# Performance work log

Hardware: AMD Instinct MI355X
Metric: run time of the kernel (lower is better)

The kernel has to match this reference:

```python
import jax, jax.numpy as jnp
import numpy as np

B, C, H, W = 4, 64, 128, 128
EPS = 1e-5


def setup_inputs() -> dict:
    key = jax.random.key(0)
    ks = jax.random.split(key, 6)
    x = jax.random.normal(ks[0], (B, C, H, W), jnp.float32)
    W1 = jax.random.normal(ks[1], (C, C), jnp.float32) * 0.1
    b1 = jnp.zeros((C,), jnp.float32)
    W2 = jax.random.normal(ks[2], (C, C), jnp.float32) * 0.1
    b2 = jnp.zeros((C,), jnp.float32)
    Wc = jax.random.normal(ks[3], (C, C, 3, 3), jnp.float32) * 0.05
    bn_w = jnp.ones((C,), jnp.float32)
    bn_b = jnp.zeros((C,), jnp.float32)
    gamma = jax.random.normal(ks[4], (1,), jnp.float32) * 0.5
    return dict(x=x, W1=W1, b1=b1, W2=W2, b2=b2, Wc=Wc, bn_w=bn_w, bn_b=bn_b, gamma=gamma)


def reference(x, W1, b1, W2, b2, Wc, bn_w, bn_b, gamma):
    b, c, h, w = x.shape
    # feat_h: [B,W,C,H] flattened to [C, B*W, H] (exact torch .view semantics)
    feat_h = x.transpose(0, 3, 1, 2).reshape(c, b * w, h)
    # feat_w: [B,H,C,W] flattened to [C, B*H, W]
    feat_w = x.transpose(0, 2, 1, 3).reshape(c, b * h, w)
    # avg-pool over W -> [B,C,H] -> [C,H,B]; 1x1 conv == channel mix on dim0
    enc_h = jnp.einsum('oi,ihb->ohb', W1, x.mean(axis=3).transpose(1, 2, 0)) + b1[:, None, None]  # [C,H,B]
    enc_w = jnp.einsum('oi,iwb->owb', W2, x.mean(axis=2).transpose(1, 2, 0)) + b2[:, None, None]  # [C,W,B]
    # energy_h: [C, B*W, B*W]
    energy_h = jnp.matmul(feat_h, jnp.tile(enc_h, (1, 1, w)))
    rel_h = jax.nn.softmax(energy_h, axis=-1)
    aug_h = jnp.matmul(rel_h, feat_h).reshape(b, w, c, h).transpose(0, 2, 3, 1)  # [B,C,H,W]
    # energy_w: [C, B*H, B*H]
    energy_w = jnp.matmul(feat_w, jnp.tile(enc_w, (1, 1, h)))
    rel_w = jax.nn.softmax(energy_w, axis=-1)
    aug_w = jnp.matmul(rel_w, feat_w).reshape(b, h, c, w).transpose(0, 2, 1, 3)  # [B,C,H,W]
    out = gamma * (aug_h + aug_w) + x
    # 3x3 conv (no bias) + BatchNorm2d (training-mode batch stats) + ReLU
    y = jax.lax.conv_general_dilated(out, Wc, (1, 1), 'SAME',
                                     dimension_numbers=('NCHW', 'OIHW', 'NCHW'))
    mean = y.mean(axis=(0, 2, 3), keepdims=True)
    var = y.var(axis=(0, 2, 3), keepdims=True)
    y = (y - mean) * jax.lax.rsqrt(var + EPS)
    y = y * bn_w[None, :, None, None] + bn_b[None, :, None, None]
    return jax.nn.relu(y)
```

## Files before the change

### kernel.cpp

```cpp
#include <hip/hip_runtime.h>
#include <math.h>

#define BDIM 4
#define CDIM 64
#define HDIM 128
#define WDIM 128
#define PLANE (HDIM*WDIM)
#define CHW (CDIM*PLANE)

typedef unsigned short ushort_t;
typedef short short8 __attribute__((ext_vector_type(8)));
typedef float floatx4 __attribute__((ext_vector_type(4)));

__device__ inline unsigned int pack_bf16(float lo, float hi) {
  unsigned int ul = __float_as_uint(lo);
  unsigned int uh = __float_as_uint(hi);
  unsigned int rl = (ul + 0x7FFFu + ((ul >> 16) & 1u)) >> 16;
  unsigned int rh = (uh + 0x7FFFu + ((uh >> 16) & 1u)) >> 16;
  return (rh << 16) | (rl & 0xFFFFu);
}

__global__ __launch_bounds__(256) void k1_T_rowmean(const float* __restrict__ x,
                                                    float* __restrict__ T,
                                                    float* __restrict__ xmw) {
  int bid = blockIdx.x;
  int b = bid >> 7, h = bid & 127;
  int t = threadIdx.x;
  int wid = t >> 6, lane = t & 63;
  const float* xp = x + (size_t)b * CHW + h * WDIM;
  float tr[4] = {0,0,0,0}, ur[4] = {0,0,0,0};
#pragma unroll
  for (int cc = 0; cc < 16; cc++) {
    int c = wid * 16 + cc;
    int k = cc & 3;
    float v0 = xp[c * PLANE + lane];
    float v1 = xp[c * PLANE + lane + 64];
    tr[k] += v0; ur[k] += v1;
    float s = v0 + v1;
#pragma unroll
    for (int off = 32; off; off >>= 1) s += __shfl_xor(s, off);
    if (lane == 0) xmw[(b * CDIM + c) * HDIM + h] = s * (1.f / WDIM);
  }
  __shared__ float4 pt[4][128];
  pt[wid][lane]      = make_float4(tr[0], tr[1], tr[2], tr[3]);
  pt[wid][lane + 64] = make_float4(ur[0], ur[1], ur[2], ur[3]);
  __syncthreads();
  if (t < 128) {
    float4 a = pt[0][t], bb = pt[1][t], cvec = pt[2][t], d = pt[3][t];
    float4 s = make_float4(a.x + bb.x + cvec.x + d.x, a.y + bb.y + cvec.y + d.y,
                           a.z + bb.z + cvec.z + d.z, a.w + bb.w + cvec.w + d.w);
    ((float4*)T)[(b * HDIM + h) * WDIM + t] = s;
  }
}

__global__ void k2_colmean(const float* __restrict__ x, float* __restrict__ xmh) {
  int bid = blockIdx.x;
  int b = bid >> 6, c = bid & 63;
  int t = threadIdx.x;
  int tw = t & 127, th2 = t >> 7;
  const float* xp = x + (size_t)(b * CDIM + c) * PLANE;
  float s = 0.f;
  for (int h = th2 * 64; h < th2 * 64 + 64; h++) s += xp[h * WDIM + tw];
  __shared__ float sh[256];
  sh[t] = s;
  __syncthreads();
  if (t < 128) xmh[(b * CDIM + c) * WDIM + t] = (sh[t] + sh[t + 128]) * (1.f / HDIM);
}

__global__ void k3_enc(const float* __restrict__ W1, const float* __restrict__ bias1,
                       const float* __restrict__ W2, const float* __restrict__ bias2,
                       const float* __restrict__ xmw, const float* __restrict__ xmh,
                       float* __restrict__ ench, float* __restrict__ encw) {
  int bid = blockIdx.x;
  int t = threadIdx.x;
  int o = t >> 2, bb = t & 3;
  if (bid < HDIM) {
    int h = bid;
    float s = bias1[o];
    for (int i = 0; i < CDIM; i++) s += W1[o * CDIM + i] * xmw[(bb * CDIM + i) * HDIM + h];
    ench[(o * HDIM + h) * 4 + bb] = s;
  } else {
    int w = bid - HDIM;
    float s = bias2[o];
    for (int i = 0; i < CDIM; i++) s += W2[o * CDIM + i] * xmh[(bb * CDIM + i) * WDIM + w];
    encw[(o * WDIM + w) * 4 + bb] = s;
  }
}

__global__ __launch_bounds__(256) void k4_probs(const float* __restrict__ x,
                                                const float* __restrict__ ench,
                                                const float* __restrict__ encw,
                                                float* __restrict__ Ph,
                                                float* __restrict__ Pw) {
  __shared__ float plane[HDIM * WDIM];
  int bid = blockIdx.x;
  int b = bid >> 6, c = bid & 63;
  int t = threadIdx.x;
  const float* xp = x + (size_t)(b * CDIM + c) * PLANE;
#pragma unroll 4
  for (int j = 0; j < 64; j++) {
    int idx = j * 256 + t;
    int row = idx >> 7, col = idx & 127;
    plane[row * WDIM + (col ^ (row & 31))] = xp[idx];
  }
  __syncthreads();
  int half = t >> 7, p = t & 127;
  int c2 = (b * HDIM + p) >> 3;
  float e0 = 0, e1 = 0, e2 = 0, e3 = 0;
  if (half == 0) {
    const float4* E = (const float4*)ench + c2 * HDIM;
    for (int h = 0; h < HDIM; h++) {
      float v = plane[h * WDIM + (p ^ (h & 31))];
      float4 e = E[h];
      e0 += v * e.x; e1 += v * e.y; e2 += v * e.z; e3 += v * e.w;
    }
  } else {
    const float4* E = (const float4*)encw + c2 * WDIM;
    for (int w = 0; w < WDIM; w++) {
      float v = plane[p * WDIM + (w ^ (p & 31))];
      float4 e = E[w];
      e0 += v * e.x; e1 += v * e.y; e2 += v * e.z; e3 += v * e.w;
    }
  }
  float m = fmaxf(fmaxf(e0, e1), fmaxf(e2, e3));
  float p0 = expf(e0 - m), p1 = expf(e1 - m), p2 = expf(e2 - m), p3 = expf(e3 - m);
  float sc = 1.f / ((p0 + p1 + p2 + p3) * 128.f);
  float4* dst = (half == 0) ? (float4*)Ph : (float4*)Pw;
  dst[c2 * 512 + (p & 7) * 64 + c] = make_float4(p0 * sc, p1 * sc, p2 * sc, p3 * sc);
}

__global__ void k4b_groups(const float* __restrict__ T, float* __restrict__ Gh,
                           float* __restrict__ Gw) {
  int c2 = blockIdx.x;
  int t = threadIdx.x;
  int b = c2 >> 4;
  int w0 = (c2 & 15) * 8;
  const float4* T4 = (const float4*)T;
  float4 s = make_float4(0, 0, 0, 0);
#pragma unroll
  for (int dw = 0; dw < 8; dw++) {
    float4 v = T4[(b * HDIM + t) * WDIM + w0 + dw];
    s.x += v.x; s.y += v.y; s.z += v.z; s.w += v.w;
  }
  ((float4*)Gh)[c2 * HDIM + t] = s;
  float4 s2 = make_float4(0, 0, 0, 0);
#pragma unroll
  for (int dh = 0; dh < 8; dh++) {
    float4 v = T4[(b * HDIM + w0 + dh) * WDIM + t];
    s2.x += v.x; s2.y += v.y; s2.z += v.z; s2.w += v.w;
  }
  ((float4*)Gw)[c2 * WDIM + t] = s2;
}

__global__ __launch_bounds__(256) void k5_out(const float* __restrict__ x,
                                              const float* __restrict__ Ph,
                                              const float* __restrict__ Pw,
                                              const float* __restrict__ Gh,
                                              const float* __restrict__ Gw,
                                              const float* __restrict__ gamma,
                                              float* __restrict__ outb) {
  int bid = blockIdx.x;
  int hq = bid & 3, c = (bid >> 2) & 63, b = bid >> 8;
  int t = threadIdx.x;
  int tw = t & 127, th2 = t >> 7;
  float g = gamma[0];
  int c2h = (b * HDIM + tw) >> 3;
  float4 ph = ((const float4*)Ph)[c2h * 512 + (tw & 7) * 64 + c];
  const float* xp = x + (size_t)(b * CDIM + c) * PLANE;
  float* op = outb + (size_t)(b * CDIM + c) * PLANE;
#pragma unroll 4
  for (int j = 0; j < 16; j++) {
    int h = hq * 32 + j * 2 + th2;
    int c2w = (b * HDIM + h) >> 3;
    float4 pw = ((const float4*)Pw)[c2w * 512 + (h & 7) * 64 + c];
    float4 gh = ((const float4*)Gh)[c2h * HDIM + h];
    float4 gw = ((const float4*)Gw)[c2w * WDIM + tw];
    float val = ph.x * gh.x + ph.y * gh.y + ph.z * gh.z + ph.w * gh.w
              + pw.x * gw.x + pw.y * gw.y + pw.z * gw.z + pw.w * gw.w;
    op[h * WDIM + tw] = fmaf(g, val, xp[h * WDIM + tw]);
  }
}

__global__ void k6_prep(const float* __restrict__ Wc, ushort_t* __restrict__ afrag) {
  int idx = blockIdx.x * 256 + threadIdx.x;
  if (idx >= 4608) return;
  int lane = idx & 63;
  int m = (idx >> 6) & 3;
  int chunk = (idx >> 8) & 1;
  int tap = idx >> 9;
  int dh = tap / 3, dw = tap % 3;
  int o = m * 16 + (lane & 15);
  int ib = chunk * 32 + (lane >> 4) * 8;
  unsigned int d[4];
#pragma unroll
  for (int j = 0; j < 4; j++) {
    float lo = Wc[((size_t)(o * CDIM + ib + 2 * j) * 3 + dh) * 3 + dw];
    float hi = Wc[((size_t)(o * CDIM + ib + 2 * j + 1) * 3 + dh) * 3 + dw];
    d[j] = pack_bf16(lo, hi);
  }
  uint4* dst = (uint4*)afrag + idx;
  *dst = make_uint4(d[0], d[1], d[2], d[3]);
}

__global__ __launch_bounds__(512) void k6_conv(const float* __restrict__ outb,
                                               const ushort_t* __restrict__ afrag,
                                               float* __restrict__ yb) {
  __shared__ uint4 lds_in[3 * 130 * 4];
  int bid = blockIdx.x;
  int b = bid >> 7, h0 = bid & 127;
  int t = threadIdx.x;
  int lane = t & 63, wv = t >> 6;
  int w0 = wv * 16;
  const float* inb = outb + (size_t)b * CHW;

  floatx4 acc[4];
#pragma unroll
  for (int m = 0; m < 4; m++) acc[m] = (floatx4){0.f, 0.f, 0.f, 0.f};

  for (int chunk = 0; chunk < 2; chunk++) {
    int i0 = chunk * 32;
    __syncthreads();
#pragma unroll
    for (int k = 0; k < 4; k++) {
      int gid = k * 512 + t;
      if (gid < 1560) {
        int wlp = gid % 130;
        int rest = gid / 130;
        int g = rest & 3, lr = rest >> 2;
        int h = h0 - 1 + lr, wl = wlp - 1;
        unsigned int d0 = 0, d1 = 0, d2 = 0, d3 = 0;
        if (h >= 0 && h < HDIM && wl >= 0 && wl < WDIM) {
          const float* sp = inb + (size_t)(i0 + g * 8) * PLANE + h * WDIM + wl;
          float v0 = sp[0], v1 = sp[PLANE], v2 = sp[2 * PLANE], v3 = sp[3 * PLANE];
          float v4 = sp[4 * PLANE], v5 = sp[5 * PLANE], v6 = sp[6 * PLANE], v7 = sp[7 * PLANE];
          d0 = pack_bf16(v0, v1); d1 = pack_bf16(v2, v3);
          d2 = pack_bf16(v4, v5); d3 = pack_bf16(v6, v7);
        }
        int pg = g ^ ((wlp >> 1) & 3);
        lds_in[(lr * 130 + wlp) * 4 + pg] = make_uint4(d0, d1, d2, d3);
      }
    }
    __syncthreads();
#pragma unroll
    for (int tap = 0; tap < 9; tap++) {
      int lr = tap / 3, dw = tap % 3;
      int wlp = w0 + (lane & 15) + dw;
      int pg = (lane >> 4) ^ ((wlp >> 1) & 3);
      short8 bf = *(const short8*)&lds_in[(lr * 130 + wlp) * 4 + pg];
      const short8* ap = (const short8*)afrag + (size_t)((tap * 2 + chunk) * 4) * 64 + lane;
#pragma unroll
      for (int m = 0; m < 4; m++) {
        short8 a = ap[m * 64];
        acc[m] = __builtin_amdgcn_mfma_f32_16x16x32_bf16(a, bf, acc[m], 0, 0, 0);
      }
    }
  }
  int col = lane & 15, rg = lane >> 4;
#pragma unroll
  for (int m = 0; m < 4; m++) {
#pragma unroll
    for (int j = 0; j < 4; j++) {
      int o = m * 16 + rg * 4 + j;
      yb[((size_t)(b * CDIM + o) * HDIM + h0) * WDIM + w0 + col] = acc[m][j];
    }
  }
}

__global__ __launch_bounds__(512) void k7a_stats(const float* __restrict__ yb,
                                                 float* __restrict__ part) {
  int bid = blockIdx.x;
  int t = threadIdx.x;
  const float4* yp = (const float4*)(yb + (size_t)bid * PLANE);
  float s = 0.f, ss = 0.f;
  for (int r = t; r < PLANE / 4; r += 512) {
    float4 v = yp[r];
    s  += v.x + v.y + v.z + v.w;
    ss += v.x * v.x + v.y * v.y + v.z * v.z + v.w * v.w;
  }
#pragma unroll
  for (int off = 32; off; off >>= 1) { s += __shfl_xor(s, off); ss += __shfl_xor(ss, off); }
  __shared__ float sh[16];
  int wid = t >> 6;
  if ((t & 63) == 0) { sh[wid] = s; sh[8 + wid] = ss; }
  __syncthreads();
  if (t == 0) {
    s = 0.f; ss = 0.f;
#pragma unroll
    for (int wv = 0; wv < 8; wv++) { s += sh[wv]; ss += sh[8 + wv]; }
    part[bid] = s;
    part[256 + bid] = ss;
  }
}

__global__ void k7b_finalize(const float* __restrict__ part, float* __restrict__ stats) {
  int o = threadIdx.x;
  float s = 0.f, ss = 0.f;
#pragma unroll
  for (int b = 0; b < BDIM; b++) { s += part[b * 64 + o]; ss += part[256 + b * 64 + o]; }
  float n = (float)(BDIM * PLANE);
  float m = s / n;
  float var = ss / n - m * m;
  stats[o] = m;
  stats[64 + o] = rsqrtf(var + 1e-5f);
}

__global__ void k8_norm(const float* __restrict__ yb, const float* __restrict__ stats,
                        const float* __restrict__ bnw, const float* __restrict__ bnb,
                        float* __restrict__ out) {
  int idx = blockIdx.x * 256 + threadIdx.x;
  int c = (idx >> 12) & 63;
  float4 v = ((const float4*)yb)[idx];
  float m = stats[c], rs = stats[64 + c], w = bnw[c], bb = bnb[c];
  v.x = fmaxf(0.f, (v.x - m) * rs * w + bb);
  v.y = fmaxf(0.f, (v.y - m) * rs * w + bb);
  v.z = fmaxf(0.f, (v.z - m) * rs * w + bb);
  v.w = fmaxf(0.f, (v.w - m) * rs * w + bb);
  ((float4*)out)[idx] = v;
}

extern "C" void kernel_launch(void* const* d_in, const int* in_sizes, int n_in,
                              void* d_out, int out_size, void* d_ws, size_t ws_size,
                              hipStream_t stream) {
  const float* x     = (const float*)d_in[0];
  const float* W1    = (const float*)d_in[1];
  const float* b1    = (const float*)d_in[2];
  const float* W2    = (const float*)d_in[3];
  const float* b2    = (const float*)d_in[4];
  const float* Wc    = (const float*)d_in[5];
  const float* bnw   = (const float*)d_in[6];
  const float* bnb   = (const float*)d_in[7];
  const float* gamma = (const float*)d_in[8];
  float* out = (float*)d_out;

  float* ws   = (float*)d_ws;
  float* T    = ws;
  float* xmw  = T    + 262144;
  float* xmh  = xmw  + 32768;
  float* ench = xmh  + 32768;
  float* encw = ench + 32768;
  float* Ph   = encw + 32768;
  float* Pw   = Ph   + 131072;
  float* Gh   = Pw   + 131072;
  float* Gw   = Gh   + 32768;
  float* outb = Gw   + 32768;
  float* yb   = outb + 4194304;
  float* part = yb   + 4194304;
  float* stats= part + 512;
  ushort_t* afrag = (ushort_t*)(stats + 128);

  k6_prep     <<<18, 256, 0, stream>>>(Wc, afrag);
  k1_T_rowmean<<<512, 256, 0, stream>>>(x, T, xmw);
  k2_colmean  <<<256, 256, 0, stream>>>(x, xmh);
  k3_enc      <<<256, 256, 0, stream>>>(W1, b1, W2, b2, xmw, xmh, ench, encw);
  k4_probs    <<<256, 256, 0, stream>>>(x, ench, encw, Ph, Pw);
  k4b_groups  <<<64, 128, 0, stream>>>(T, Gh, Gw);
  k5_out      <<<1024, 256, 0, stream>>>(x, Ph, Pw, Gh, Gw, gamma, outb);
  k6_conv     <<<512, 512, 0, stream>>>(outb, afrag, yb);
  k7a_stats   <<<256, 512, 0, stream>>>(yb, part);
  k7b_finalize<<<1, 64, 0, stream>>>(part, stats);
  k8_norm     <<<4096, 256, 0, stream>>>(yb, stats, bnw, bnb, out);
}
```

Before: 171.0 us.

## Fuse attention output into conv loader, BN stats into conv epilogue, merge small kernels

The residual attention output is no longer written to a buffer. The conv input loader now recomputes gamma*(Ph·Gh+Pw·Gw)+x directly while staging bf16 tiles, which removes a full 16 MB write and read. BatchNorm statistics are gathered in the conv epilogue with shuffles, shared atomics and global atomics, which drops the separate stats and finalize kernels; the encoder and group-sum kernels are also merged and k4_probs splits its reductions across 512 threads. In exchange the conv loader does more redundant arithmetic and gathers per halo element, and the float atomics make the statistics order nondeterministic.

```diff
diff --git a/kernel.cpp b/kernel.cpp
--- a/kernel.cpp
+++ b/kernel.cpp
@@ -67,122 +67,103 @@
   if (t < 128) xmh[(b * CDIM + c) * WDIM + t] = (sh[t] + sh[t + 128]) * (1.f / HDIM);
 }
 
-__global__ void k3_enc(const float* __restrict__ W1, const float* __restrict__ bias1,
-                       const float* __restrict__ W2, const float* __restrict__ bias2,
-                       const float* __restrict__ xmw, const float* __restrict__ xmh,
-                       float* __restrict__ ench, float* __restrict__ encw) {
-  int bid = blockIdx.x;
-  int t = threadIdx.x;
-  int o = t >> 2, bb = t & 3;
-  if (bid < HDIM) {
-    int h = bid;
-    float s = bias1[o];
-    for (int i = 0; i < CDIM; i++) s += W1[o * CDIM + i] * xmw[(bb * CDIM + i) * HDIM + h];
-    ench[(o * HDIM + h) * 4 + bb] = s;
-  } else {
-    int w = bid - HDIM;
-    float s = bias2[o];
-    for (int i = 0; i < CDIM; i++) s += W2[o * CDIM + i] * xmh[(bb * CDIM + i) * WDIM + w];
-    encw[(o * WDIM + w) * 4 + bb] = s;
-  }
-}
-
-__global__ __launch_bounds__(256) void k4_probs(const float* __restrict__ x,
+__global__ void k3_enc_groups(const float* __restrict__ W1, const float* __restrict__ bias1,
+                              const float* __restrict__ W2, const float* __restrict__ bias2,
+                              const float* __restrict__ xmw, const float* __restrict__ xmh,
+                              const float* __restrict__ T,
+                              float* __restrict__ ench, float* __restrict__ encw,
+                              float* __restrict__ Gh, float* __restrict__ Gw) {
+  int bid = blockIdx.x;
+  int t = threadIdx.x;
+  if (bid < 256) {
+    int o = t >> 2, bb = t & 3;
+    if (bid < HDIM) {
+      int h = bid;
+      float s = bias1[o];
+      for (int i = 0; i < CDIM; i++) s += W1[o * CDIM + i] * xmw[(bb * CDIM + i) * HDIM + h];
+      ench[(o * HDIM + h) * 4 + bb] = s;
+    } else {
+      int w = bid - HDIM;
+      float s = bias2[o];
+      for (int i = 0; i < CDIM; i++) s += W2[o * CDIM + i] * xmh[(bb * CDIM + i) * WDIM + w];
+      encw[(o * WDIM + w) * 4 + bb] = s;
+    }
+  } else if (t < 128) {
+    int c2 = bid - 256;
+    int b = c2 >> 4;
+    int w0 = (c2 & 15) * 8;
+    const float4* T4 = (const float4*)T;
+    float4 s = make_float4(0, 0, 0, 0);
+#pragma unroll
+    for (int dw = 0; dw < 8; dw++) {
+      float4 v = T4[(b * HDIM + t) * WDIM + w0 + dw];
+      s.x += v.x; s.y += v.y; s.z += v.z; s.w += v.w;
+    }
+    ((float4*)Gh)[c2 * HDIM + t] = s;
+    float4 s2 = make_float4(0, 0, 0, 0);
+#pragma unroll
+    for (int dh = 0; dh < 8; dh++) {
+      float4 v = T4[(b * HDIM + w0 + dh) * WDIM + t];
+      s2.x += v.x; s2.y += v.y; s2.z += v.z; s2.w += v.w;
+    }
+    ((float4*)Gw)[c2 * WDIM + t] = s2;
+  }
+}
+
+__global__ __launch_bounds__(512) void k4_probs(const float* __restrict__ x,
                                                 const float* __restrict__ ench,
                                                 const float* __restrict__ encw,
                                                 float* __restrict__ Ph,
                                                 float* __restrict__ Pw) {
   __shared__ float plane[HDIM * WDIM];
+  __shared__ float4 esh[512];
   int bid = blockIdx.x;
   int b = bid >> 6, c = bid & 63;
   int t = threadIdx.x;
   const float* xp = x + (size_t)(b * CDIM + c) * PLANE;
 #pragma unroll 4
-  for (int j = 0; j < 64; j++) {
-    int idx = j * 256 + t;
+  for (int j = 0; j < 32; j++) {
+    int idx = j * 512 + t;
     int row = idx >> 7, col = idx & 127;
     plane[row * WDIM + (col ^ (row & 31))] = xp[idx];
   }
   __syncthreads();
-  int half = t >> 7, p = t & 127;
+  int q = t >> 7, p = t & 127;
+  int branch = q >> 1, seg = q & 1;
   int c2 = (b * HDIM + p) >> 3;
   float e0 = 0, e1 = 0, e2 = 0, e3 = 0;
-  if (half == 0) {
+  if (branch == 0) {
     const float4* E = (const float4*)ench + c2 * HDIM;
-    for (int h = 0; h < HDIM; h++) {
+    for (int h = seg * 64; h < seg * 64 + 64; h++) {
       float v = plane[h * WDIM + (p ^ (h & 31))];
       float4 e = E[h];
       e0 += v * e.x; e1 += v * e.y; e2 += v * e.z; e3 += v * e.w;
     }
   } else {
     const float4* E = (const float4*)encw + c2 * WDIM;
-    for (int w = 0; w < WDIM; w++) {
+    for (int w = seg * 64; w < seg * 64 + 64; w++) {
       float v = plane[p * WDIM + (w ^ (p & 31))];
       float4 e = E[w];
       e0 += v * e.x; e1 += v * e.y; e2 += v * e.z; e3 += v * e.w;
     }
   }
-  float m = fmaxf(fmaxf(e0, e1), fmaxf(e2, e3));
-  float p0 = expf(e0 - m), p1 = expf(e1 - m), p2 = expf(e2 - m), p3 = expf(e3 - m);
-  float sc = 1.f / ((p0 + p1 + p2 + p3) * 128.f);
-  float4* dst = (half == 0) ? (float4*)Ph : (float4*)Pw;
-  dst[c2 * 512 + (p & 7) * 64 + c] = make_float4(p0 * sc, p1 * sc, p2 * sc, p3 * sc);
-}
-
-__global__ void k4b_groups(const float* __restrict__ T, float* __restrict__ Gh,
-                           float* __restrict__ Gw) {
-  int c2 = blockIdx.x;
-  int t = threadIdx.x;
-  int b = c2 >> 4;
-  int w0 = (c2 & 15) * 8;
-  const float4* T4 = (const float4*)T;
-  float4 s = make_float4(0, 0, 0, 0);
-#pragma unroll
-  for (int dw = 0; dw < 8; dw++) {
-    float4 v = T4[(b * HDIM + t) * WDIM + w0 + dw];
-    s.x += v.x; s.y += v.y; s.z += v.z; s.w += v.w;
-  }
-  ((float4*)Gh)[c2 * HDIM + t] = s;
-  float4 s2 = make_float4(0, 0, 0, 0);
-#pragma unroll
-  for (int dh = 0; dh < 8; dh++) {
-    float4 v = T4[(b * HDIM + w0 + dh) * WDIM + t];
-    s2.x += v.x; s2.y += v.y; s2.z += v.z; s2.w += v.w;
-  }
-  ((float4*)Gw)[c2 * WDIM + t] = s2;
-}
-
-__global__ __launch_bounds__(256) void k5_out(const float* __restrict__ x,
-                                              const float* __restrict__ Ph,
-                                              const float* __restrict__ Pw,
-                                              const float* __restrict__ Gh,
-                                              const float* __restrict__ Gw,
-                                              const float* __restrict__ gamma,
-                                              float* __restrict__ outb) {
-  int bid = blockIdx.x;
-  int hq = bid & 3, c = (bid >> 2) & 63, b = bid >> 8;
-  int t = threadIdx.x;
-  int tw = t & 127, th2 = t >> 7;
-  float g = gamma[0];
-  int c2h = (b * HDIM + tw) >> 3;
-  float4 ph = ((const float4*)Ph)[c2h * 512 + (tw & 7) * 64 + c];
-  const float* xp = x + (size_t)(b * CDIM + c) * PLANE;
-  float* op = outb + (size_t)(b * CDIM + c) * PLANE;
-#pragma unroll 4
-  for (int j = 0; j < 16; j++) {
-    int h = hq * 32 + j * 2 + th2;
-    int c2w = (b * HDIM + h) >> 3;
-    float4 pw = ((const float4*)Pw)[c2w * 512 + (h & 7) * 64 + c];
-    float4 gh = ((const float4*)Gh)[c2h * HDIM + h];
-    float4 gw = ((const float4*)Gw)[c2w * WDIM + tw];
-    float val = ph.x * gh.x + ph.y * gh.y + ph.z * gh.z + ph.w * gh.w
-              + pw.x * gw.x + pw.y * gw.y + pw.z * gw.z + pw.w * gw.w;
-    op[h * WDIM + tw] = fmaf(g, val, xp[h * WDIM + tw]);
-  }
-}
-
-__global__ void k6_prep(const float* __restrict__ Wc, ushort_t* __restrict__ afrag) {
+  esh[t] = make_float4(e0, e1, e2, e3);
+  __syncthreads();
+  if (seg == 0) {
+    float4 o = esh[t + 128];
+    e0 += o.x; e1 += o.y; e2 += o.z; e3 += o.w;
+    float m = fmaxf(fmaxf(e0, e1), fmaxf(e2, e3));
+    float p0 = __expf(e0 - m), p1 = __expf(e1 - m), p2 = __expf(e2 - m), p3 = __expf(e3 - m);
+    float sc = 1.f / ((p0 + p1 + p2 + p3) * 128.f);
+    float4* dst = (branch == 0) ? (float4*)Ph : (float4*)Pw;
+    dst[c2 * 512 + (p & 7) * 64 + c] = make_float4(p0 * sc, p1 * sc, p2 * sc, p3 * sc);
+  }
+}
+
+__global__ void k6_prep(const float* __restrict__ Wc, ushort_t* __restrict__ afrag,
+                        float* __restrict__ part) {
   int idx = blockIdx.x * 256 + threadIdx.x;
+  if (idx < 128) part[idx] = 0.f;
   if (idx >= 4608) return;
   int lane = idx & 63;
   int m = (idx >> 6) & 3;
@@ -202,16 +183,30 @@
   *dst = make_uint4(d[0], d[1], d[2], d[3]);
 }
 
-__global__ __launch_bounds__(512) void k6_conv(const float* __restrict__ outb,
+__global__ __launch_bounds__(512) void k6_conv(const float* __restrict__ x,
+                                               const float* __restrict__ Ph,
+                                               const float* __restrict__ Pw,
+                                               const float* __restrict__ Gh,
+                                               const float* __restrict__ Gw,
+                                               const float* __restrict__ gamma,
                                                const ushort_t* __restrict__ afrag,
-                                               float* __restrict__ yb) {
+                                               float* __restrict__ yb,
+                                               float* __restrict__ part) {
   __shared__ uint4 lds_in[3 * 130 * 4];
+  __shared__ float sh_s[64], sh_ss[64];
   int bid = blockIdx.x;
   int b = bid >> 7, h0 = bid & 127;
   int t = threadIdx.x;
   int lane = t & 63, wv = t >> 6;
   int w0 = wv * 16;
-  const float* inb = outb + (size_t)b * CHW;
+  const float* xb = x + (size_t)b * CHW;
+  const float4* Ph4 = (const float4*)Ph;
+  const float4* Pw4 = (const float4*)Pw;
+  const float4* Gh4 = (const float4*)Gh;
+  const float4* Gw4 = (const float4*)Gw;
+  float gm = gamma[0];
+
+  if (t < 64) { sh_s[t] = 0.f; sh_ss[t] = 0.f; }
 
   floatx4 acc[4];
 #pragma unroll
@@ -230,11 +225,24 @@
         int h = h0 - 1 + lr, wl = wlp - 1;
         unsigned int d0 = 0, d1 = 0, d2 = 0, d3 = 0;
         if (h >= 0 && h < HDIM && wl >= 0 && wl < WDIM) {
-          const float* sp = inb + (size_t)(i0 + g * 8) * PLANE + h * WDIM + wl;
-          float v0 = sp[0], v1 = sp[PLANE], v2 = sp[2 * PLANE], v3 = sp[3 * PLANE];
-          float v4 = sp[4 * PLANE], v5 = sp[5 * PLANE], v6 = sp[6 * PLANE], v7 = sp[7 * PLANE];
-          d0 = pack_bf16(v0, v1); d1 = pack_bf16(v2, v3);
-          d2 = pack_bf16(v4, v5); d3 = pack_bf16(v6, v7);
+          int c0 = i0 + g * 8;
+          int c2h = (b * HDIM + wl) >> 3;
+          int c2w = (b * HDIM + h) >> 3;
+          float4 gh4 = Gh4[c2h * HDIM + h];
+          float4 gw4 = Gw4[c2w * WDIM + wl];
+          const float4* php = Ph4 + c2h * 512 + (wl & 7) * 64 + c0;
+          const float4* pwp = Pw4 + c2w * 512 + (h & 7) * 64 + c0;
+          const float* xpp = xb + (size_t)c0 * PLANE + h * WDIM + wl;
+          float v[8];
+#pragma unroll
+          for (int j = 0; j < 8; j++) {
+            float4 ph = php[j], pw = pwp[j];
+            float val = ph.x * gh4.x + ph.y * gh4.y + ph.z * gh4.z + ph.w * gh4.w
+                      + pw.x * gw4.x + pw.y * gw4.y + pw.z * gw4.z + pw.w * gw4.w;
+            v[j] = fmaf(gm, val, xpp[j * PLANE]);
+          }
+          d0 = pack_bf16(v[0], v[1]); d1 = pack_bf16(v[2], v[3]);
+          d2 = pack_bf16(v[4], v[5]); d3 = pack_bf16(v[6], v[7]);
         }
         int pg = g ^ ((wlp >> 1) & 3);
         lds_in[(lr * 130 + wlp) * 4 + pg] = make_uint4(d0, d1, d2, d3);
@@ -261,60 +269,51 @@
 #pragma unroll
     for (int j = 0; j < 4; j++) {
       int o = m * 16 + rg * 4 + j;
-      yb[((size_t)(b * CDIM + o) * HDIM + h0) * WDIM + w0 + col] = acc[m][j];
-    }
-  }
-}
-
-__global__ __launch_bounds__(512) void k7a_stats(const float* __restrict__ yb,
-                                                 float* __restrict__ part) {
-  int bid = blockIdx.x;
-  int t = threadIdx.x;
-  const float4* yp = (const float4*)(yb + (size_t)bid * PLANE);
-  float s = 0.f, ss = 0.f;
-  for (int r = t; r < PLANE / 4; r += 512) {
-    float4 v = yp[r];
-    s  += v.x + v.y + v.z + v.w;
-    ss += v.x * v.x + v.y * v.y + v.z * v.z + v.w * v.w;
-  }
-#pragma unroll
-  for (int off = 32; off; off >>= 1) { s += __shfl_xor(s, off); ss += __shfl_xor(ss, off); }
-  __shared__ float sh[16];
-  int wid = t >> 6;
-  if ((t & 63) == 0) { sh[wid] = s; sh[8 + wid] = ss; }
-  __syncthreads();
-  if (t == 0) {
-    s = 0.f; ss = 0.f;
-#pragma unroll
-    for (int wv = 0; wv < 8; wv++) { s += sh[wv]; ss += sh[8 + wv]; }
-    part[bid] = s;
-    part[256 + bid] = ss;
-  }
-}
-
-__global__ void k7b_finalize(const float* __restrict__ part, float* __restrict__ stats) {
-  int o = threadIdx.x;
-  float s = 0.f, ss = 0.f;
-#pragma unroll
-  for (int b = 0; b < BDIM; b++) { s += part[b * 64 + o]; ss += part[256 + b * 64 + o]; }
-  float n = (float)(BDIM * PLANE);
-  float m = s / n;
-  float var = ss / n - m * m;
-  stats[o] = m;
-  stats[64 + o] = rsqrtf(var + 1e-5f);
-}
-
-__global__ void k8_norm(const float* __restrict__ yb, const float* __restrict__ stats,
-                        const float* __restrict__ bnw, const float* __restrict__ bnb,
-                        float* __restrict__ out) {
-  int idx = blockIdx.x * 256 + threadIdx.x;
+      float v = acc[m][j];
+      yb[((size_t)(b * CDIM + o) * HDIM + h0) * WDIM + w0 + col] = v;
+      float vs = v, vq = v * v;
+#pragma unroll
+      for (int off = 1; off < 16; off <<= 1) {
+        vs += __shfl_xor(vs, off);
+        vq += __shfl_xor(vq, off);
+      }
+      if (col == 0) {
+        atomicAdd(&sh_s[o], vs);
+        atomicAdd(&sh_ss[o], vq);
+      }
+    }
+  }
+  __syncthreads();
+  if (t < 64) {
+    atomicAdd(&part[t], sh_s[t]);
+    atomicAdd(&part[64 + t], sh_ss[t]);
+  }
+}
+
+__global__ __launch_bounds__(256) void k8_norm(const float* __restrict__ yb,
+                                               const float* __restrict__ part,
+                                               const float* __restrict__ bnw,
+                                               const float* __restrict__ bnb,
+                                               float* __restrict__ out) {
+  __shared__ float sa[64], sb2[64];
+  int t = threadIdx.x;
+  if (t < 64) {
+    float s = part[t], ss = part[64 + t];
+    float m = s * (1.f / 65536.f);
+    float var = ss * (1.f / 65536.f) - m * m;
+    float a = rsqrtf(var + 1e-5f) * bnw[t];
+    sa[t] = a;
+    sb2[t] = bnb[t] - m * a;
+  }
+  __syncthreads();
+  int idx = blockIdx.x * 256 + t;
   int c = (idx >> 12) & 63;
   float4 v = ((const float4*)yb)[idx];
-  float m = stats[c], rs = stats[64 + c], w = bnw[c], bb = bnb[c];
-  v.x = fmaxf(0.f, (v.x - m) * rs * w + bb);
-  v.y = fmaxf(0.f, (v.y - m) * rs * w + bb);
-  v.z = fmaxf(0.f, (v.z - m) * rs * w + bb);
-  v.w = fmaxf(0.f, (v.w - m) * rs * w + bb);
+  float a = sa[c], bb = sb2[c];
+  v.x = fmaxf(0.f, v.x * a + bb);
+  v.y = fmaxf(0.f, v.y * a + bb);
+  v.z = fmaxf(0.f, v.z * a + bb);
+  v.w = fmaxf(0.f, v.w * a + bb);
   ((float4*)out)[idx] = v;
 }
 
@@ -342,21 +341,15 @@
   float* Pw   = Ph   + 131072;
   float* Gh   = Pw   + 131072;
   float* Gw   = Gh   + 32768;
-  float* outb = Gw   + 32768;
-  float* yb   = outb + 4194304;
+  float* yb   = Gw   + 32768;
   float* part = yb   + 4194304;
-  float* stats= part + 512;
-  ushort_t* afrag = (ushort_t*)(stats + 128);
-
-  k6_prep     <<<18, 256, 0, stream>>>(Wc, afrag);
-  k1_T_rowmean<<<512, 256, 0, stream>>>(x, T, xmw);
-  k2_colmean  <<<256, 256, 0, stream>>>(x, xmh);
-  k3_enc      <<<256, 256, 0, stream>>>(W1, b1, W2, b2, xmw, xmh, ench, encw);
-  k4_probs    <<<256, 256, 0, stream>>>(x, ench, encw, Ph, Pw);
-  k4b_groups  <<<64, 128, 0, stream>>>(T, Gh, Gw);
-  k5_out      <<<1024, 256, 0, stream>>>(x, Ph, Pw, Gh, Gw, gamma, outb);
-  k6_conv     <<<512, 512, 0, stream>>>(outb, afrag, yb);
-  k7a_stats   <<<256, 512, 0, stream>>>(yb, part);
-  k7b_finalize<<<1, 64, 0, stream>>>(part, stats);
-  k8_norm     <<<4096, 256, 0, stream>>>(yb, stats, bnw, bnb, out);
-}
+  ushort_t* afrag = (ushort_t*)(part + 128);
+
+  k6_prep       <<<18, 256, 0, stream>>>(Wc, afrag, part);
+  k1_T_rowmean  <<<512, 256, 0, stream>>>(x, T, xmw);
+  k2_colmean    <<<256, 256, 0, stream>>>(x, xmh);
+  k3_enc_groups <<<320, 256, 0, stream>>>(W1, b1, W2, b2, xmw, xmh, T, ench, encw, Gh, Gw);
+  k4_probs      <<<256, 512, 0, stream>>>(x, ench, encw, Ph, Pw);
+  k6_conv       <<<512, 512, 0, stream>>>(x, Ph, Pw, Gh, Gw, gamma, afrag, yb, part);
+  k8_norm       <<<4096, 256, 0, stream>>>(yb, part, bnw, bnb, out);
+}
```

Result: slower. 186.0 us (+8.8%).
